# Kernel optimization log

Hardware: AMD Instinct MI355X
Metric: run time of the kernel (lower is better)

The kernel has to match this reference:

```python
import jax, jax.numpy as jnp
import numpy as np

N = 100000      # nodes
E = 3200000     # edges (before self-loops)
F_IN = 1433
H1, D1 = 8, 8   # layer1: 8 heads, 8 dims each -> concat 64
H2, D2 = 1, 7   # layer2: 1 head, 7 classes
NEG_SLOPE = 0.2


def setup_inputs() -> dict:
    key = jax.random.key(0)
    ks = jax.random.split(key, 10)
    x = jax.random.normal(ks[0], (N, F_IN), dtype=jnp.float32)
    edge_index = jax.random.randint(ks[1], (2, E), 0, N, dtype=jnp.int32)
    W1 = jax.random.normal(ks[2], (F_IN, H1 * D1), dtype=jnp.float32) * np.float32(1.0 / np.sqrt(F_IN))
    a1_src = jax.random.normal(ks[3], (H1, D1), dtype=jnp.float32) * 0.1
    a1_dst = jax.random.normal(ks[4], (H1, D1), dtype=jnp.float32) * 0.1
    b1 = jnp.zeros((H1 * D1,), dtype=jnp.float32)
    W2 = jax.random.normal(ks[5], (H1 * D1, H2 * D2), dtype=jnp.float32) * np.float32(1.0 / np.sqrt(H1 * D1))
    a2_src = jax.random.normal(ks[6], (H2, D2), dtype=jnp.float32) * 0.1
    a2_dst = jax.random.normal(ks[7], (H2, D2), dtype=jnp.float32) * 0.1
    b2 = jnp.zeros((D2,), dtype=jnp.float32)
    return {"x": x, "edge_index": edge_index, "W1": W1, "a1_src": a1_src,
            "a1_dst": a1_dst, "b1": b1, "W2": W2, "a2_src": a2_src,
            "a2_dst": a2_dst, "b2": b2}


def gat_layer(x, src, dst, W, a_s, a_d, b, concat):
    n = x.shape[0]
    H, D = a_s.shape
    h = (x @ W).reshape(n, H, D)                       # [N, H, D] projected features
    alpha_s = jnp.einsum('nhd,hd->nh', h, a_s)         # [N, H]
    alpha_d = jnp.einsum('nhd,hd->nh', h, a_d)
    e = jax.nn.leaky_relu(alpha_s[src] + alpha_d[dst], NEG_SLOPE)  # [E, H]
    # scatter-softmax over edges grouped by destination node
    m = jax.ops.segment_max(e, dst, num_segments=n)
    e = jnp.exp(e - m[dst])
    s = jax.ops.segment_sum(e, dst, num_segments=n)
    alpha = e / (s[dst] + 1e-16)                       # [E, H]
    msg = h[src] * alpha[:, :, None]                   # [E, H, D]
    out = jax.ops.segment_sum(msg, dst, num_segments=n)  # [N, H, D]
    out = out.reshape(n, H * D) if concat else out.mean(axis=1)
    return out + b


def reference(x, edge_index, W1, a1_src, a1_dst, b1, W2, a2_src, a2_dst, b2):
    n = x.shape[0]
    loops = jnp.arange(n, dtype=edge_index.dtype)
    src = jnp.concatenate([edge_index[0], loops])      # add self-loops (PyG default)
    dst = jnp.concatenate([edge_index[1], loops])
    h = jax.nn.relu(gat_layer(x, src, dst, W1, a1_src, a1_dst, b1, concat=True))
    # F.dropout is a no-op in eval mode
    h = gat_layer(h, src, dst, W2, a2_src, a2_dst, b2, concat=False)
    return jax.nn.log_softmax(h, axis=1)
```

## Files before the change

### kernel.cpp

```cpp
#include <hip/hip_runtime.h>

#define NN 100000
#define FIN 1433
#define KSTEPS 45
#define CAP 96
#define NBIN 391
#define BCAP 8704

typedef __attribute__((ext_vector_type(8))) short s16x8;
typedef __attribute__((ext_vector_type(4))) float f32x4;

__device__ __forceinline__ short f2bf(float f){
  unsigned u = __float_as_uint(f);
  unsigned r = (u + 0x7fffu + ((u >> 16) & 1u)) >> 16;
  return (short)r;
}
__device__ __forceinline__ float bflo(unsigned u){ return __uint_as_float(u << 16); }
__device__ __forceinline__ float bfhi(unsigned u){ return __uint_as_float(u & 0xffff0000u); }

__device__ __forceinline__ f32x4 mfma16(s16x8 a, s16x8 b, f32x4 c){
  return __builtin_amdgcn_mfma_f32_16x16x32_bf16(a, b, c, 0, 0, 0);
}

__global__ void w1pack_k(const float* __restrict__ W1, short* __restrict__ pack,
                         int* __restrict__ cursor){
  if (blockIdx.x == 45){
    for (int j = threadIdx.x; j < NBIN; j += 256) cursor[j] = 0;
    return;
  }
  int unit = blockIdx.x * 4 + (threadIdx.x >> 6);
  if (unit < KSTEPS * 4){
    int ks = unit >> 2, nf = unit & 3, l = threadIdx.x & 63;
    int col = nf * 16 + (l & 15);
    s16x8 v;
    #pragma unroll
    for (int j = 0; j < 8; j++){
      int k = ks * 32 + ((l >> 4) * 8) + j;
      float f = (k < FIN) ? W1[k * 64 + col] : 0.0f;
      v[j] = f2bf(f);
    }
    *(s16x8*)&pack[((size_t)unit * 64 + l) * 8] = v;
  }
}

__global__ void pass1_k(const int* __restrict__ srcs, const int* __restrict__ dsts,
                        int* __restrict__ cursor, uint2* __restrict__ ebuf, int E8){
  __shared__ int cntB[NBIN];
  __shared__ int baseB[NBIN];
  int t = threadIdx.x;
  for (int j = t; j < NBIN; j += 256) cntB[j] = 0;
  __syncthreads();
  int i = blockIdx.x * 256 + t;
  int sv[8], dv[8], rk[8];
  bool act = i < E8;
  if (act){
    int4 s0 = ((const int4*)srcs)[2 * i], s1 = ((const int4*)srcs)[2 * i + 1];
    int4 d0 = ((const int4*)dsts)[2 * i], d1 = ((const int4*)dsts)[2 * i + 1];
    sv[0]=s0.x; sv[1]=s0.y; sv[2]=s0.z; sv[3]=s0.w;
    sv[4]=s1.x; sv[5]=s1.y; sv[6]=s1.z; sv[7]=s1.w;
    dv[0]=d0.x; dv[1]=d0.y; dv[2]=d0.z; dv[3]=d0.w;
    dv[4]=d1.x; dv[5]=d1.y; dv[6]=d1.z; dv[7]=d1.w;
    #pragma unroll
    for (int j = 0; j < 8; j++) rk[j] = atomicAdd(&cntB[dv[j] >> 8], 1);
  }
  __syncthreads();
  for (int j = t; j < NBIN; j += 256){
    int c = cntB[j];
    baseB[j] = c ? atomicAdd(&cursor[j], c) : 0;
  }
  __syncthreads();
  if (act){
    #pragma unroll
    for (int j = 0; j < 8; j++){
      int bin = dv[j] >> 8;
      int pos = baseB[bin] + rk[j];
      if (pos < BCAP) ebuf[(size_t)bin * BCAP + pos] = make_uint2((unsigned)sv[j], (unsigned)dv[j]);
    }
  }
}

__global__ __launch_bounds__(256, 4) void k2_k(const float* __restrict__ x,
                                               const short* __restrict__ w1p,
                                               unsigned short* __restrict__ h1b,
                                               const float* __restrict__ a1s,
                                               const float* __restrict__ a1d,
                                               float* __restrict__ as1,
                                               float* __restrict__ ad1,
                                               int n, int Ggemm,
                                               const int* __restrict__ cursor,
                                               const uint2* __restrict__ ebuf,
                                               int* __restrict__ cnt,
                                               int* __restrict__ colv){
  __shared__ float lds[4][2][16][36];
  __shared__ int lcnt[256];
  if (blockIdx.x >= Ggemm){
    int bin = blockIdx.x - Ggemm;
    int t = threadIdx.x;
    int n0 = bin << 8;
    int node = n0 + t;
    bool valid = node < n;
    lcnt[t] = 1;
    if (valid) colv[(size_t)node * CAP] = node;
    __syncthreads();
    int ec = min(cursor[bin], BCAP);
    const uint2* eb = ebuf + (size_t)bin * BCAP;
    for (int i = t; i < ec; i += 256){
      uint2 e = eb[i];
      int p = atomicAdd(&lcnt[(int)e.y - n0], 1);
      if (p < CAP) colv[(size_t)e.y * CAP + p] = (int)e.x;
    }
    __syncthreads();
    if (valid) cnt[node] = lcnt[t];
    return;
  }
  int tid = threadIdx.x;
  int wid = tid >> 6, lane = tid & 63;
  int row0 = blockIdx.x * 64 + wid * 16;
  f32x4 acc[4] = {};

  int lr = lane >> 5, lc = lane & 31;
  const float* pj[8];
  #pragma unroll
  for (int j = 0; j < 8; j++){
    int rg = min(row0 + j * 2 + lr, n - 1);
    pj[j] = x + (size_t)rg * FIN + lc;
  }
  int frow = lane & 15, fg = lane >> 4;
  const s16x8* pb = ((const s16x8*)w1p) + lane;

  float rB[8], rC[8];
  {
    float rA[8];
    #pragma unroll
    for (int j = 0; j < 8; j++) rA[j] = pj[j][0];
    #pragma unroll
    for (int j = 0; j < 8; j++) rB[j] = pj[j][32];
    float (&b0)[16][36] = lds[wid][0];
    #pragma unroll
    for (int j = 0; j < 8; j++) b0[j * 2 + lr][lc] = rA[j];
  }

  #pragma unroll 2
  for (int ks = 0; ks <= 44; ks++){
    int ld = ks + 2;
    if (ld < 44){
      #pragma unroll
      for (int j = 0; j < 8; j++) rC[j] = pj[j][ld * 32];
    } else if (ld == 44){
      int toff = (lc < 25) ? 44 * 32 : 0;
      #pragma unroll
      for (int j = 0; j < 8; j++){
        float v = pj[j][toff];
        rC[j] = (lc < 25) ? v : 0.0f;
      }
    }
    if (ks < 44){
      float (&bufn)[16][36] = lds[wid][(ks + 1) & 1];
      #pragma unroll
      for (int j = 0; j < 8; j++) bufn[j * 2 + lr][lc] = rB[j];
    }
    float (&buf)[16][36] = lds[wid][ks & 1];
    f32x4 lo = *(const f32x4*)&buf[frow][fg * 8];
    f32x4 hi = *(const f32x4*)&buf[frow][fg * 8 + 4];
    s16x8 a0;
    #pragma unroll
    for (int j = 0; j < 4; j++){ a0[j] = f2bf(lo[j]); a0[j + 4] = f2bf(hi[j]); }
    s16x8 b0 = pb[(ks * 4 + 0) * 64];
    s16x8 b1 = pb[(ks * 4 + 1) * 64];
    s16x8 b2 = pb[(ks * 4 + 2) * 64];
    s16x8 b3 = pb[(ks * 4 + 3) * 64];
    acc[0] = mfma16(a0, b0, acc[0]);
    acc[1] = mfma16(a0, b1, acc[1]);
    acc[2] = mfma16(a0, b2, acc[2]);
    acc[3] = mfma16(a0, b3, acc[3]);
    #pragma unroll
    for (int j = 0; j < 8; j++) rB[j] = rC[j];
  }

  #pragma unroll
  for (int r4 = 0; r4 < 4; r4++){
    int m = row0 + (lane >> 4) * 4 + r4;
    if (m < n){
      #pragma unroll
      for (int nf = 0; nf < 4; nf++){
        float v = acc[nf][r4];
        float pv = __shfl_xor(v, 1);
        if ((lane & 1) == 0){
          unsigned pk = (unsigned)(unsigned short)f2bf(v) |
                        ((unsigned)(unsigned short)f2bf(pv) << 16);
          *(unsigned*)&h1b[(size_t)m * 64 + nf * 16 + (lane & 15)] = pk;
        }
      }
    }
  }

  int p = lane & 15;
  float cs[4], cd[4];
  #pragma unroll
  for (int nf = 0; nf < 4; nf++){
    cs[nf] = a1s[nf * 16 + p];
    cd[nf] = a1d[nf * 16 + p];
  }
  int b = (lane >> 3) & 1;
  #pragma unroll
  for (int r4 = 0; r4 < 4; r4++){
    int m = row0 + (lane >> 4) * 4 + r4;
    float s[4], d[4];
    #pragma unroll
    for (int nf = 0; nf < 4; nf++){
      s[nf] = acc[nf][r4] * cs[nf];
      d[nf] = acc[nf][r4] * cd[nf];
      s[nf] += __shfl_xor(s[nf], 1); d[nf] += __shfl_xor(d[nf], 1);
      s[nf] += __shfl_xor(s[nf], 2); d[nf] += __shfl_xor(d[nf], 2);
      s[nf] += __shfl_xor(s[nf], 4); d[nf] += __shfl_xor(d[nf], 4);
    }
    if ((lane & 7) == 0 && m < n){
      #pragma unroll
      for (int nf = 0; nf < 4; nf++){
        as1[m * 8 + 2 * nf + b] = s[nf];
        ad1[m * 8 + 2 * nf + b] = d[nf];
      }
    }
  }
}

__global__ void agg1_k(const int* __restrict__ cnt, const int* __restrict__ colv,
                       const unsigned short* __restrict__ h1b,
                       const float* __restrict__ as1, const float* __restrict__ ad1,
                       const float* __restrict__ b1, const float* __restrict__ W2,
                       const float* __restrict__ a2s, const float* __restrict__ a2d,
                       float* __restrict__ h2, float* __restrict__ vs2,
                       float* __restrict__ vd2, int n){
  int node = blockIdx.x * 4 + (threadIdx.x >> 6);
  if (node >= n) return;
  int l = threadIdx.x & 63, sl = l & 7, qw = l >> 3;
  float adn = ad1[node * 8 + sl];
  float a[8] = {0,0,0,0,0,0,0,0};
  float sw = 0.0f;
  int beg = node * CAP, end = beg + min(cnt[node], CAP);
  for (int i = beg + qw; i < end; i += 8){
    int s0 = colv[i];
    float e0 = as1[s0 * 8 + sl] + adn;
    uint4 u = *(const uint4*)(h1b + (size_t)s0 * 64 + 8 * sl);
    e0 = e0 > 0.0f ? e0 : 0.2f * e0;
    float w0 = __expf(e0);
    a[0] += w0 * bflo(u.x); a[1] += w0 * bfhi(u.x);
    a[2] += w0 * bflo(u.y); a[3] += w0 * bfhi(u.y);
    a[4] += w0 * bflo(u.z); a[5] += w0 * bfhi(u.z);
    a[6] += w0 * bflo(u.w); a[7] += w0 * bfhi(u.w);
    sw += w0;
  }
  sw += __shfl_xor(sw, 8); sw += __shfl_xor(sw, 16); sw += __shfl_xor(sw, 32);
  #pragma unroll
  for (int j = 0; j < 8; j++){
    a[j] += __shfl_xor(a[j], 8);
    a[j] += __shfl_xor(a[j], 16);
    a[j] += __shfl_xor(a[j], 32);
  }

  float inv = 1.0f / (sw + 1e-16f);
  float4 bv0 = *(const float4*)&b1[8 * sl];
  float4 bv1 = *(const float4*)&b1[8 * sl + 4];
  float o[8];
  o[0] = a[0] * inv + bv0.x; o[1] = a[1] * inv + bv0.y;
  o[2] = a[2] * inv + bv0.z; o[3] = a[3] * inv + bv0.w;
  o[4] = a[4] * inv + bv1.x; o[5] = a[5] * inv + bv1.y;
  o[6] = a[6] * inv + bv1.z; o[7] = a[7] * inv + bv1.w;
  #pragma unroll
  for (int j = 0; j < 8; j++) o[j] = o[j] > 0.0f ? o[j] : 0.0f;

  const float* wr = W2 + 56 * sl;
  float dot[7];
  #pragma unroll
  for (int c = 0; c < 7; c++){
    float s = 0.0f;
    #pragma unroll
    for (int j = 0; j < 8; j++) s += o[j] * wr[7 * j + c];
    dot[c] = s;
  }
  #pragma unroll
  for (int c = 0; c < 7; c++){
    dot[c] += __shfl_xor(dot[c], 1);
    dot[c] += __shfl_xor(dot[c], 2);
    dot[c] += __shfl_xor(dot[c], 4);
  }
  if (l < 7) h2[(size_t)node * 7 + l] = dot[l];
  if (l == 0){
    float s = 0.0f, d = 0.0f;
    #pragma unroll
    for (int c = 0; c < 7; c++){
      s += dot[c] * a2s[c];
      d += dot[c] * a2d[c];
    }
    vs2[node] = s; vd2[node] = d;
  }
}

__global__ void agg2_k(const int* __restrict__ cnt, const int* __restrict__ colv,
                       const float* __restrict__ h2, const float* __restrict__ vs2,
                       const float* __restrict__ vd2, const float* __restrict__ b2,
                       float* __restrict__ out, int n){
  int node = blockIdx.x * 4 + (threadIdx.x >> 6);
  if (node >= n) return;
  int l = threadIdx.x & 63, c = l & 7, qw = l >> 3;
  bool cls = c < 7;
  float adn = vd2[node];
  float acc = 0.0f, sw = 0.0f;
  int beg = node * CAP, end = beg + min(cnt[node], CAP);
  int i = beg + qw;
  for (; i + 8 < end; i += 16){
    int s0 = colv[i], s1 = colv[i + 8];
    float e0 = vs2[s0] + adn;
    float e1 = vs2[s1] + adn;
    float v0 = cls ? h2[(size_t)s0 * 7 + c] : 0.0f;
    float v1 = cls ? h2[(size_t)s1 * 7 + c] : 0.0f;
    e0 = e0 > 0.0f ? e0 : 0.2f * e0;
    e1 = e1 > 0.0f ? e1 : 0.2f * e1;
    float w0 = __expf(e0), w1 = __expf(e1);
    acc += w0 * v0 + w1 * v1;
    sw += w0 + w1;
  }
  if (i < end){
    int s0 = colv[i];
    float e0 = vs2[s0] + adn;
    e0 = e0 > 0.0f ? e0 : 0.2f * e0;
    float w0 = __expf(e0);
    acc += w0 * (cls ? h2[(size_t)s0 * 7 + c] : 0.0f);
    sw += w0;
  }
  acc += __shfl_xor(acc, 8);  acc += __shfl_xor(acc, 16); acc += __shfl_xor(acc, 32);
  sw  += __shfl_xor(sw, 8);   sw  += __shfl_xor(sw, 16);  sw  += __shfl_xor(sw, 32);
  if (qw == 0){
    float inv = 1.0f / (sw + 1e-16f);
    float o = cls ? acc * inv + b2[c] : -1e30f;
    float m = o;
    m = fmaxf(m, __shfl_xor(m, 1, 8));
    m = fmaxf(m, __shfl_xor(m, 2, 8));
    m = fmaxf(m, __shfl_xor(m, 4, 8));
    float ex = cls ? __expf(o - m) : 0.0f;
    float s8 = ex;
    s8 += __shfl_xor(s8, 1, 8);
    s8 += __shfl_xor(s8, 2, 8);
    s8 += __shfl_xor(s8, 4, 8);
    if (cls) out[(size_t)node * 7 + c] = o - m - __logf(s8);
  }
}

extern "C" void kernel_launch(void* const* d_in, const int* in_sizes, int n_in,
                              void* d_out, int out_size, void* d_ws, size_t ws_size,
                              hipStream_t stream){
  const float* x   = (const float*)d_in[0];
  const int*   ei  = (const int*)d_in[1];
  const float* W1  = (const float*)d_in[2];
  const float* a1s = (const float*)d_in[3];
  const float* a1d = (const float*)d_in[4];
  const float* b1  = (const float*)d_in[5];
  const float* W2  = (const float*)d_in[6];
  const float* a2s = (const float*)d_in[7];
  const float* a2d = (const float*)d_in[8];
  const float* b2  = (const float*)d_in[9];
  int E = in_sizes[1] / 2;
  const int* srcs = ei;
  const int* dsts = ei + E;
  int n = in_sizes[0] / FIN;

  char* ws = (char*)d_ws;
  size_t off = 0;
  auto alloc = [&](size_t bytes)->void*{
    void* p = ws + off; off += (bytes + 255) & ~(size_t)255; return p;
  };
  unsigned short* h1b = (unsigned short*)alloc((size_t)n * 64 * 2);
  float* as1  = (float*)alloc((size_t)n * 8 * 4);
  float* ad1  = (float*)alloc((size_t)n * 8 * 4);
  float* h2   = (float*)alloc((size_t)n * 7 * 4);
  float* vs2  = (float*)alloc((size_t)n * 4);
  float* vd2  = (float*)alloc((size_t)n * 4);
  int* cnt    = (int*)alloc((size_t)(n + 256) * 4);
  int* colv   = (int*)alloc((size_t)n * CAP * 4);
  short* w1p  = (short*)alloc((size_t)KSTEPS * 4 * 64 * 8 * 2);
  uint2* ebuf = (uint2*)alloc((size_t)NBIN * BCAP * 8);
  int* cursor = (int*)alloc((size_t)NBIN * 4);
  (void)ws_size; (void)n_in; (void)out_size;

  int E8 = E / 8;
  int Gp1 = (E8 + 255) / 256;
  int Ggemm = (n + 63) / 64;

  w1pack_k<<<46, 256, 0, stream>>>(W1, w1p, cursor);
  pass1_k<<<Gp1, 256, 0, stream>>>(srcs, dsts, cursor, ebuf, E8);
  k2_k<<<Ggemm + NBIN, 256, 0, stream>>>(x, w1p, h1b, a1s, a1d, as1, ad1,
                                         n, Ggemm, cursor, ebuf, cnt, colv);
  agg1_k<<<(n + 3) / 4, 256, 0, stream>>>(cnt, colv, h1b, as1, ad1, b1,
                                          W2, a2s, a2d, h2, vs2, vd2, n);
  agg2_k<<<(n + 3) / 4, 256, 0, stream>>>(cnt, colv, h2, vs2, vd2, b2,
                                          (float*)d_out, n);
}
```

Before: 478.0 us.

## Stream x tiles directly into LDS with triple-buffered global_load_lds in GEMM

Replaces the register-staged double-buffered load of x in the layer-1 projection GEMM with 16-byte global_load_lds transfers into a three-stage, XOR-swizzled per-wave LDS ring. It also prefetches the packed W1 fragments one k-step ahead, and uses explicit vmcnt waits with scheduling barriers to overlap loads with MFMA work. The aim is to cut VGPR traffic and instruction overhead on the bandwidth-bound read of x. The risks are that the hand-counted waitcnt values and the unaligned 16-byte row accesses (each row is 1433 floats) must be correct. The final partial k-step now uses a separate scalar path.

```diff
diff --git a/kernel.cpp b/kernel.cpp
--- a/kernel.cpp
+++ b/kernel.cpp
@@ -20,6 +20,12 @@
 
 __device__ __forceinline__ f32x4 mfma16(s16x8 a, s16x8 b, f32x4 c){
   return __builtin_amdgcn_mfma_f32_16x16x32_bf16(a, b, c, 0, 0, 0);
+}
+
+__device__ __forceinline__ void gload16(const float* g, f32x4* l){
+  __builtin_amdgcn_global_load_lds((const __attribute__((address_space(1))) void*)g,
+                                   (__attribute__((address_space(3))) void*)l,
+                                   16, 0, 0);
 }
 
 __global__ void w1pack_k(const float* __restrict__ W1, short* __restrict__ pack,
@@ -91,7 +97,7 @@
                                                const uint2* __restrict__ ebuf,
                                                int* __restrict__ cnt,
                                                int* __restrict__ colv){
-  __shared__ float lds[4][2][16][36];
+  __shared__ f32x4 ldsb[4][3][128];
   __shared__ int lcnt[256];
   if (blockIdx.x >= Ggemm){
     int bin = blockIdx.x - Ggemm;
@@ -118,63 +124,107 @@
   int row0 = blockIdx.x * 64 + wid * 16;
   f32x4 acc[4] = {};
 
-  int lr = lane >> 5, lc = lane & 31;
-  const float* pj[8];
-  #pragma unroll
-  for (int j = 0; j < 8; j++){
-    int rg = min(row0 + j * 2 + lr, n - 1);
-    pj[j] = x + (size_t)rg * FIN + lc;
-  }
+  int lr8 = lane >> 3;
+  int cs  = (lane & 7) ^ lr8;
+  int rg0 = min(row0 + lr8, n - 1);
+  int rg1 = min(row0 + 8 + lr8, n - 1);
+  const float* g0 = x + (size_t)rg0 * FIN + cs * 4;
+  const float* g1 = x + (size_t)rg1 * FIN + cs * 4;
+
   int frow = lane & 15, fg = lane >> 4;
+  int ci_lo = frow * 8 + 2 * (fg ^ ((frow >> 1) & 3)) + (frow & 1);
+  int ci_hi = ci_lo ^ 1;
+
   const s16x8* pb = ((const s16x8*)w1p) + lane;
-
-  float rB[8], rC[8];
+  f32x4* w0 = &ldsb[wid][0][0];
+  f32x4* w1 = &ldsb[wid][1][0];
+  f32x4* w2 = &ldsb[wid][2][0];
+
+  gload16(g0, w0); gload16(g1, w0 + 64);
+  s16x8 bc0 = pb[0 * 64], bc1 = pb[1 * 64], bc2 = pb[2 * 64], bc3 = pb[3 * 64];
+  gload16(g0 + 32, w1); gload16(g1 + 32, w1 + 64);
+
+  #pragma unroll 3
+  for (int ks = 0; ks < 42; ks++){
+    s16x8 bn0 = pb[((ks + 1) * 4 + 0) * 64];
+    s16x8 bn1 = pb[((ks + 1) * 4 + 1) * 64];
+    s16x8 bn2 = pb[((ks + 1) * 4 + 2) * 64];
+    s16x8 bn3 = pb[((ks + 1) * 4 + 3) * 64];
+    f32x4* bw = (ks % 3 == 0) ? w2 : ((ks % 3 == 1) ? w0 : w1);
+    gload16(g0 + (ks + 2) * 32, bw);
+    gload16(g1 + (ks + 2) * 32, bw + 64);
+    asm volatile("s_waitcnt vmcnt(8)" ::: "memory");
+    __builtin_amdgcn_sched_barrier(0);
+    f32x4* br = (ks % 3 == 0) ? w0 : ((ks % 3 == 1) ? w1 : w2);
+    f32x4 lo = br[ci_lo];
+    f32x4 hi = br[ci_hi];
+    s16x8 a0;
+    #pragma unroll
+    for (int j = 0; j < 4; j++){ a0[j] = f2bf(lo[j]); a0[j + 4] = f2bf(hi[j]); }
+    acc[0] = mfma16(a0, bc0, acc[0]);
+    acc[1] = mfma16(a0, bc1, acc[1]);
+    acc[2] = mfma16(a0, bc2, acc[2]);
+    acc[3] = mfma16(a0, bc3, acc[3]);
+    bc0 = bn0; bc1 = bn1; bc2 = bn2; bc3 = bn3;
+  }
   {
-    float rA[8];
-    #pragma unroll
-    for (int j = 0; j < 8; j++) rA[j] = pj[j][0];
-    #pragma unroll
-    for (int j = 0; j < 8; j++) rB[j] = pj[j][32];
-    float (&b0)[16][36] = lds[wid][0];
-    #pragma unroll
-    for (int j = 0; j < 8; j++) b0[j * 2 + lr][lc] = rA[j];
-  }
-
-  #pragma unroll 2
-  for (int ks = 0; ks <= 44; ks++){
-    int ld = ks + 2;
-    if (ld < 44){
-      #pragma unroll
-      for (int j = 0; j < 8; j++) rC[j] = pj[j][ld * 32];
-    } else if (ld == 44){
-      int toff = (lc < 25) ? 44 * 32 : 0;
-      #pragma unroll
-      for (int j = 0; j < 8; j++){
-        float v = pj[j][toff];
-        rC[j] = (lc < 25) ? v : 0.0f;
-      }
-    }
-    if (ks < 44){
-      float (&bufn)[16][36] = lds[wid][(ks + 1) & 1];
-      #pragma unroll
-      for (int j = 0; j < 8; j++) bufn[j * 2 + lr][lc] = rB[j];
-    }
-    float (&buf)[16][36] = lds[wid][ks & 1];
-    f32x4 lo = *(const f32x4*)&buf[frow][fg * 8];
-    f32x4 hi = *(const f32x4*)&buf[frow][fg * 8 + 4];
+    s16x8 bn0 = pb[(43 * 4 + 0) * 64];
+    s16x8 bn1 = pb[(43 * 4 + 1) * 64];
+    s16x8 bn2 = pb[(43 * 4 + 2) * 64];
+    s16x8 bn3 = pb[(43 * 4 + 3) * 64];
+    asm volatile("s_waitcnt vmcnt(6)" ::: "memory");
+    __builtin_amdgcn_sched_barrier(0);
+    f32x4 lo = w0[ci_lo];
+    f32x4 hi = w0[ci_hi];
     s16x8 a0;
     #pragma unroll
     for (int j = 0; j < 4; j++){ a0[j] = f2bf(lo[j]); a0[j + 4] = f2bf(hi[j]); }
-    s16x8 b0 = pb[(ks * 4 + 0) * 64];
-    s16x8 b1 = pb[(ks * 4 + 1) * 64];
-    s16x8 b2 = pb[(ks * 4 + 2) * 64];
-    s16x8 b3 = pb[(ks * 4 + 3) * 64];
-    acc[0] = mfma16(a0, b0, acc[0]);
-    acc[1] = mfma16(a0, b1, acc[1]);
-    acc[2] = mfma16(a0, b2, acc[2]);
-    acc[3] = mfma16(a0, b3, acc[3]);
-    #pragma unroll
-    for (int j = 0; j < 8; j++) rB[j] = rC[j];
+    acc[0] = mfma16(a0, bc0, acc[0]);
+    acc[1] = mfma16(a0, bc1, acc[1]);
+    acc[2] = mfma16(a0, bc2, acc[2]);
+    acc[3] = mfma16(a0, bc3, acc[3]);
+    bc0 = bn0; bc1 = bn1; bc2 = bn2; bc3 = bn3;
+  }
+  {
+    s16x8 bn0 = pb[(44 * 4 + 0) * 64];
+    s16x8 bn1 = pb[(44 * 4 + 1) * 64];
+    s16x8 bn2 = pb[(44 * 4 + 2) * 64];
+    s16x8 bn3 = pb[(44 * 4 + 3) * 64];
+    asm volatile("s_waitcnt vmcnt(4)" ::: "memory");
+    __builtin_amdgcn_sched_barrier(0);
+    f32x4 lo = w1[ci_lo];
+    f32x4 hi = w1[ci_hi];
+    s16x8 a0;
+    #pragma unroll
+    for (int j = 0; j < 4; j++){ a0[j] = f2bf(lo[j]); a0[j + 4] = f2bf(hi[j]); }
+    acc[0] = mfma16(a0, bc0, acc[0]);
+    acc[1] = mfma16(a0, bc1, acc[1]);
+    acc[2] = mfma16(a0, bc2, acc[2]);
+    acc[3] = mfma16(a0, bc3, acc[3]);
+    bc0 = bn0; bc1 = bn1; bc2 = bn2; bc3 = bn3;
+  }
+  {
+    f32x4 t0, t1;
+    #pragma unroll
+    for (int k = 0; k < 4; k++){
+      bool ok = (cs * 4 + k) < 25;
+      int off = ok ? (44 * 32 + k) : 0;
+      float v0 = g0[off];
+      float v1 = g1[off];
+      t0[k] = ok ? v0 : 0.0f;
+      t1[k] = ok ? v1 : 0.0f;
+    }
+    w2[lane] = t0;
+    w2[64 + lane] = t1;
+    f32x4 lo = w2[ci_lo];
+    f32x4 hi = w2[ci_hi];
+    s16x8 a0;
+    #pragma unroll
+    for (int j = 0; j < 4; j++){ a0[j] = f2bf(lo[j]); a0[j + 4] = f2bf(hi[j]); }
+    acc[0] = mfma16(a0, bc0, acc[0]);
+    acc[1] = mfma16(a0, bc1, acc[1]);
+    acc[2] = mfma16(a0, bc2, acc[2]);
+    acc[3] = mfma16(a0, bc3, acc[3]);
   }
 
   #pragma unroll
@@ -195,11 +245,11 @@
   }
 
   int p = lane & 15;
-  float cs[4], cd[4];
+  float cs1[4], cd1[4];
   #pragma unroll
   for (int nf = 0; nf < 4; nf++){
-    cs[nf] = a1s[nf * 16 + p];
-    cd[nf] = a1d[nf * 16 + p];
+    cs1[nf] = a1s[nf * 16 + p];
+    cd1[nf] = a1d[nf * 16 + p];
   }
   int b = (lane >> 3) & 1;
   #pragma unroll
@@ -208,8 +258,8 @@
     float s[4], d[4];
     #pragma unroll
     for (int nf = 0; nf < 4; nf++){
-      s[nf] = acc[nf][r4] * cs[nf];
-      d[nf] = acc[nf][r4] * cd[nf];
+      s[nf] = acc[nf][r4] * cs1[nf];
+      d[nf] = acc[nf][r4] * cd1[nf];
       s[nf] += __shfl_xor(s[nf], 1); d[nf] += __shfl_xor(d[nf], 1);
       s[nf] += __shfl_xor(s[nf], 2); d[nf] += __shfl_xor(d[nf], 2);
       s[nf] += __shfl_xor(s[nf], 4); d[nf] += __shfl_xor(d[nf], 4);
```

New measurement: 470.2 us. About the same (-1.6%).
